# Performance work log

Hardware: AMD Instinct MI355X
Metric: run time of the kernel (lower is better)

The kernel has to match this reference:

```python
import jax, jax.numpy as jnp
import numpy as np

N = 50000      # nodes
E = 800000     # edges (avg degree 16)
D = 128        # embed_dim
H = 8          # nhead
HD = D // H    # head dim = 16


def setup_inputs() -> dict:
    key = jax.random.key(0)
    ks = jax.random.split(key, 6)
    s = 1.0 / np.sqrt(D)  # ~xavier scale for square matrices
    return {
        "feats": jax.random.normal(ks[0], (N, D), jnp.float32),
        "edge_index": jax.random.randint(ks[1], (E, 2), 0, N, dtype=jnp.int64),
        "Wq": jax.random.normal(ks[2], (D, D), jnp.float32) * s,
        "bq": jnp.zeros((D,), jnp.float32),
        "Wk": jax.random.normal(ks[3], (D, D), jnp.float32) * s,
        "bk": jnp.zeros((D,), jnp.float32),
        "Wv": jax.random.normal(ks[4], (D, D), jnp.float32) * s,
        "bv": jnp.zeros((D,), jnp.float32),
        "Wo": jax.random.normal(ks[5], (D, D), jnp.float32) * s,
        "bo": jnp.zeros((D,), jnp.float32),
    }


def reference(feats, edge_index, Wq, bq, Wk, bk, Wv, bv, Wo, bo):
    # Projections (nn.Linear: x @ W.T + b), split into heads: [N, H, HD]
    q = (feats @ Wq.T + bq).reshape(N, H, HD)
    k = (feats @ Wk.T + bk).reshape(N, H, HD)
    v = (feats @ Wv.T + bv).reshape(N, H, HD)

    r = edge_index[:, 0]  # source nodes
    c = edge_index[:, 1]  # destination nodes (softmax / aggregation groups)

    # Per-edge, per-head dot-product scores: [E, H]
    scores = jnp.einsum('ehd,ehd->eh', q[c], k[r]) / np.sqrt(HD)

    # Custom scatter-softmax: src_max clamped to min 0; extra exp(-src_max) in denom
    smax = jnp.maximum(jax.ops.segment_max(scores, c, num_segments=N), 0.0)  # [N, H]
    ex = jnp.exp(scores - smax[c])                                           # [E, H]
    denom = jax.ops.segment_sum(ex, c, num_segments=N)                       # [N, H]
    attn = ex / (denom + jnp.exp(-smax))[c]                                  # [E, H]

    # Weighted V per edge, scatter-mean to destination nodes
    out_e = attn[:, :, None] * v[r]                      # [E, H, HD]
    agg = jax.ops.segment_sum(out_e, c, num_segments=N)  # [N, H, HD]
    cnt = jax.ops.segment_sum(jnp.ones((E,), jnp.float32), c, num_segments=N)
    agg = agg / jnp.maximum(cnt, 1.0)[:, None, None]

    return agg.reshape(N, D) @ Wo.T + bo
```

## Files before the change

### kernel.cpp

```cpp
#include <hip/hip_runtime.h>
#include <hip/hip_bf16.h>

#define N_NODES 50000
#define N_EDGES 800000
#define DIM 128
#define NHEAD 8
#define HDIM 16
#define ELL_PAD 64
#define ELL_SLICES 391
#define ELL_BLOCKS (8 * ELL_SLICES)
#define ROWTILES 3125
#define QKV_WAVES (ROWTILES * 3)
#define QKV_GRID ((QKV_WAVES + 3) / 4)
#define OUT_WAVES (ROWTILES * 2)
#define OUT_GRID ((OUT_WAVES + 3) / 4)

#define Q_OFF      0ull
#define KV_OFF     12800000ull
#define AGG_OFF    38400000ull
#define ELL_OFF    51200000ull
#define CNT_OFF    64000000ull
#define WBF_OFF    64200192ull
#define BIAS_OFF   64331264ull

typedef __attribute__((ext_vector_type(8))) short short8;
typedef __attribute__((ext_vector_type(4))) float floatx4;

__device__ inline float bflo2f(unsigned u) { return __uint_as_float(u << 16); }
__device__ inline float bfhi2f(unsigned u) { return __uint_as_float(u & 0xffff0000u); }
__device__ inline unsigned short f2bf(float f) {
    unsigned u = __float_as_uint(f);
    return (unsigned short)((u + 0x7fffu + ((u >> 16) & 1u)) >> 16);
}

__device__ inline void detect_flags(const void* feats, const void* edge,
                                    int& isbf, int& is32) {
    const unsigned short* f = (const unsigned short*)feats;
    const unsigned int* eg = (const unsigned int*)edge;
    int lane = threadIdx.x & 63;
    unsigned e = (f[lane] >> 7) & 0xFF;
    int junk = (e >= 0x90 || (e > 0 && e <= 0x60)) ? 1 : 0;
    unsigned long long jm = __ballot(junk);
    int nz = (lane < 32 && eg[2 * lane + 1] != 0) ? 1 : 0;
    unsigned long long nm = __ballot(nz);
    isbf = (jm == 0ull) ? 1 : 0;
    is32 = (nm != 0ull) ? 1 : 0;
}

__device__ inline void load_edge(const int* edge, int is32, int e, int& r, int& c) {
    if (is32) { int2 p = ((const int2*)edge)[e]; r = p.x; c = p.y; }
    else {
        const long long* p = (const long long*)edge;
        r = (int)p[2 * e]; c = (int)p[2 * e + 1];
    }
    if ((unsigned)r >= N_NODES) r = 0;
    if ((unsigned)c >= N_NODES) c = 0;
}

__device__ inline float ldf(const void* p, int isbf, int i) {
    return isbf ? __bfloat162float(((const __hip_bfloat16*)p)[i])
                : ((const float*)p)[i];
}

__device__ inline short8 ldfrag(const void* base, int isbf, size_t off) {
    if (isbf) return *(const short8*)((const unsigned short*)base + off);
    const float* f = (const float*)base + off;
    float4 f0 = *(const float4*)f;
    float4 f1 = *(const float4*)(f + 4);
    short8 a;
    a[0] = (short)f2bf(f0.x); a[1] = (short)f2bf(f0.y);
    a[2] = (short)f2bf(f0.z); a[3] = (short)f2bf(f0.w);
    a[4] = (short)f2bf(f1.x); a[5] = (short)f2bf(f1.y);
    a[6] = (short)f2bf(f1.z); a[7] = (short)f2bf(f1.w);
    return a;
}

__global__ __launch_bounds__(256) void ell_build(const void* feats, const int* edge,
                                                 const void* wq, const void* wk,
                                                 const void* wv, const void* wo,
                                                 const void* bq, const void* bk,
                                                 const void* bv, const void* bo,
                                                 int* cnt, int* ell,
                                                 unsigned short* wbf, float* bias) {
    int isbf, is32; detect_flags(feats, edge, isbf, is32);

    if (blockIdx.x >= ELL_BLOCKS) {
        int b2 = blockIdx.x - ELL_BLOCKS;
        if (b2 == 256) {
            for (int j = threadIdx.x; j < 512; j += 256) {
                int m2 = j >> 7;
                const void* bb = (m2 == 0) ? bq : (m2 == 1) ? bk : (m2 == 2) ? bv : bo;
                bias[j] = ldf(bb, isbf, j & 127);
            }
            return;
        }
        if (isbf) return;
        int idx = b2 * 256 + (int)threadIdx.x;
        int mm = idx >> 14, rem = idx & 16383;
        const void* wsrc = (mm == 0) ? wq : (mm == 1) ? wk : (mm == 2) ? wv : wo;
        wbf[idx] = f2bf(((const float*)wsrc)[rem]);
        return;
    }

    int pid = blockIdx.x & 7, slice = blockIdx.x >> 3;
    int base = slice * 2048 + (int)threadIdx.x;
    #pragma unroll
    for (int j = 0; j < 8; ++j) {
        int e = base + j * 256;
        if (e < N_EDGES) {
            int r, c; load_edge(edge, is32, e, r, c);
            if ((c & 7) == pid) {
                int slot = atomicAdd(cnt + c, 1);
                if (slot < ELL_PAD) ell[c * ELL_PAD + slot] = r;
            }
        }
    }
}

__global__ __launch_bounds__(256) void qkv_mfma(const void* feats_raw, const int* edge,
                                                const void* wq_raw, const void* wk_raw,
                                                const void* wv_raw,
                                                const unsigned short* wbf,
                                                const float* bias,
                                                unsigned short* q_s, unsigned short* kv_s) {
    int isbf, is32; detect_flags(feats_raw, edge, isbf, is32);
    int w = blockIdx.x * 4 + (threadIdx.x >> 6);
    if (w >= QKV_WAVES) return;
    int rowtile = w / 3;
    int m = w - rowtile * 3;
    int lane = threadIdx.x & 63;
    int mrow = lane & 15, quad = lane >> 4;
    int arow = rowtile * 16 + mrow;

    short8 a[4];
    #pragma unroll
    for (int kt = 0; kt < 4; ++kt)
        a[kt] = ldfrag(feats_raw, isbf, (size_t)arow * DIM + quad * 8 + kt * 32);

    const void* wraw = (m == 0) ? wq_raw : (m == 1) ? wk_raw : wv_raw;
    const unsigned short* wm = isbf ? (const unsigned short*)wraw : wbf + m * 16384;
    int soff = (m == 2) ? 16 : 0;

    for (int nt = 0; nt < 8; ++nt) {
        float b = bias[m * 128 + nt * 16 + mrow];
        floatx4 acc = {b, b, b, b};
        const unsigned short* wp = wm + (size_t)(nt * 16 + mrow) * DIM + quad * 8;
        #pragma unroll
        for (int kt = 0; kt < 4; ++kt) {
            short8 bf = *(const short8*)(wp + kt * 32);
            acc = __builtin_amdgcn_mfma_f32_16x16x32_bf16(a[kt], bf, acc, 0, 0, 0);
        }
        if (m == 0) {
            #pragma unroll
            for (int r4 = 0; r4 < 4; ++r4) {
                int row = rowtile * 16 + quad * 4 + r4;
                q_s[(size_t)row * DIM + nt * 16 + mrow] = f2bf(acc[r4]);
            }
        } else {
            #pragma unroll
            for (int r4 = 0; r4 < 4; ++r4) {
                int row = rowtile * 16 + quad * 4 + r4;
                kv_s[(size_t)row * 256 + nt * 32 + soff + mrow] = f2bf(acc[r4]);
            }
        }
    }
}

__global__ __launch_bounds__(256) void node_agg(const int* __restrict__ cnt,
                                                const int* __restrict__ ell,
                                                const unsigned short* __restrict__ q_s,
                                                const uint4* __restrict__ kvpack,
                                                uint4* __restrict__ agg_bf) {
    int node = (blockIdx.x * 256 + threadIdx.x) >> 6;
    int lane = threadIdx.x & 63;
    if (node >= N_NODES) return;
    int e = lane >> 3, h = lane & 7;

    const uint4* qp = (const uint4*)(q_s + (size_t)node * DIM + h * HDIM);
    uint4 q0 = qp[0], q1 = qp[1];
    float qv[16];
    qv[0]  = bflo2f(q0.x); qv[1]  = bfhi2f(q0.x);
    qv[2]  = bflo2f(q0.y); qv[3]  = bfhi2f(q0.y);
    qv[4]  = bflo2f(q0.z); qv[5]  = bfhi2f(q0.z);
    qv[6]  = bflo2f(q0.w); qv[7]  = bfhi2f(q0.w);
    qv[8]  = bflo2f(q1.x); qv[9]  = bfhi2f(q1.x);
    qv[10] = bflo2f(q1.y); qv[11] = bfhi2f(q1.y);
    qv[12] = bflo2f(q1.z); qv[13] = bfhi2f(q1.z);
    qv[14] = bflo2f(q1.w); qv[15] = bfhi2f(q1.w);

    int degt = cnt[node];
    int deg = degt < ELL_PAD ? degt : ELL_PAD;
    float l = 0.f;
    float acc[16];
    #pragma unroll
    for (int i = 0; i < 16; ++i) acc[i] = 0.f;

    const int* erow = ell + node * ELL_PAD;
    for (int i0 = 0; i0 < deg; i0 += 16) {
        int i1 = i0 + e, i2 = i0 + 8 + e;
        bool ok1 = i1 < deg, ok2 = i2 < deg;
        int r1 = ok1 ? erow[i1] : 0;
        int r2 = ok2 ? erow[i2] : 0;
        const uint4* kp1 = kvpack + (size_t)r1 * 32 + h * 4;
        const uint4* kp2 = kvpack + (size_t)r2 * 32 + h * 4;
        uint4 ka1 = kp1[0], kb1 = kp1[1], va1 = kp1[2], vb1 = kp1[3];
        uint4 ka2 = kp2[0], kb2 = kp2[1], va2 = kp2[2], vb2 = kp2[3];

        float s1 = 0.f;
        s1 += bflo2f(ka1.x) * qv[0]  + bfhi2f(ka1.x) * qv[1];
        s1 += bflo2f(ka1.y) * qv[2]  + bfhi2f(ka1.y) * qv[3];
        s1 += bflo2f(ka1.z) * qv[4]  + bfhi2f(ka1.z) * qv[5];
        s1 += bflo2f(ka1.w) * qv[6]  + bfhi2f(ka1.w) * qv[7];
        s1 += bflo2f(kb1.x) * qv[8]  + bfhi2f(kb1.x) * qv[9];
        s1 += bflo2f(kb1.y) * qv[10] + bfhi2f(kb1.y) * qv[11];
        s1 += bflo2f(kb1.z) * qv[12] + bfhi2f(kb1.z) * qv[13];
        s1 += bflo2f(kb1.w) * qv[14] + bfhi2f(kb1.w) * qv[15];
        float p1 = ok1 ? __expf(s1 * 0.25f) : 0.f;
        l += p1;
        acc[0]  += p1 * bflo2f(va1.x); acc[1]  += p1 * bfhi2f(va1.x);
        acc[2]  += p1 * bflo2f(va1.y); acc[3]  += p1 * bfhi2f(va1.y);
        acc[4]  += p1 * bflo2f(va1.z); acc[5]  += p1 * bfhi2f(va1.z);
        acc[6]  += p1 * bflo2f(va1.w); acc[7]  += p1 * bfhi2f(va1.w);
        acc[8]  += p1 * bflo2f(vb1.x); acc[9]  += p1 * bfhi2f(vb1.x);
        acc[10] += p1 * bflo2f(vb1.y); acc[11] += p1 * bfhi2f(vb1.y);
        acc[12] += p1 * bflo2f(vb1.z); acc[13] += p1 * bfhi2f(vb1.z);
        acc[14] += p1 * bflo2f(vb1.w); acc[15] += p1 * bfhi2f(vb1.w);

        float s2 = 0.f;
        s2 += bflo2f(ka2.x) * qv[0]  + bfhi2f(ka2.x) * qv[1];
        s2 += bflo2f(ka2.y) * qv[2]  + bfhi2f(ka2.y) * qv[3];
        s2 += bflo2f(ka2.z) * qv[4]  + bfhi2f(ka2.z) * qv[5];
        s2 += bflo2f(ka2.w) * qv[6]  + bfhi2f(ka2.w) * qv[7];
        s2 += bflo2f(kb2.x) * qv[8]  + bfhi2f(kb2.x) * qv[9];
        s2 += bflo2f(kb2.y) * qv[10] + bfhi2f(kb2.y) * qv[11];
        s2 += bflo2f(kb2.z) * qv[12] + bfhi2f(kb2.z) * qv[13];
        s2 += bflo2f(kb2.w) * qv[14] + bfhi2f(kb2.w) * qv[15];
        float p2 = ok2 ? __expf(s2 * 0.25f) : 0.f;
        l += p2;
        acc[0]  += p2 * bflo2f(va2.x); acc[1]  += p2 * bfhi2f(va2.x);
        acc[2]  += p2 * bflo2f(va2.y); acc[3]  += p2 * bfhi2f(va2.y);
        acc[4]  += p2 * bflo2f(va2.z); acc[5]  += p2 * bfhi2f(va2.z);
        acc[6]  += p2 * bflo2f(va2.w); acc[7]  += p2 * bfhi2f(va2.w);
        acc[8]  += p2 * bflo2f(vb2.x); acc[9]  += p2 * bfhi2f(vb2.x);
        acc[10] += p2 * bflo2f(vb2.y); acc[11] += p2 * bfhi2f(vb2.y);
        acc[12] += p2 * bflo2f(vb2.z); acc[13] += p2 * bfhi2f(vb2.z);
        acc[14] += p2 * bflo2f(vb2.w); acc[15] += p2 * bfhi2f(vb2.w);
    }

    #pragma unroll
    for (int m = 8; m < 64; m <<= 1) {
        l += __shfl_xor(l, m);
        #pragma unroll
        for (int i = 0; i < 16; ++i) acc[i] += __shfl_xor(acc[i], m);
    }

    float inv = 1.0f / ((1.0f + l) * (float)(degt > 0 ? degt : 1));
    if (e == 0) {
        unsigned o[8];
        #pragma unroll
        for (int i = 0; i < 8; ++i)
            o[i] = (unsigned)f2bf(acc[2 * i] * inv) | ((unsigned)f2bf(acc[2 * i + 1] * inv) << 16);
        uint4* op = agg_bf + (size_t)node * 16 + h * 2;
        op[0] = make_uint4(o[0], o[1], o[2], o[3]);
        op[1] = make_uint4(o[4], o[5], o[6], o[7]);
    }
}

__global__ __launch_bounds__(256) void out_mfma(const unsigned short* agg_bf,
                                                const void* feats, const int* edge,
                                                const void* wo_raw,
                                                const unsigned short* wbf,
                                                const float* bias, void* out) {
    int isbf, is32; detect_flags(feats, edge, isbf, is32);
    const unsigned short* W = isbf ? (const unsigned short*)wo_raw : wbf + 3 * 16384;
    int w = blockIdx.x * 4 + (threadIdx.x >> 6);
    if (w >= OUT_WAVES) return;
    int rowtile = w >> 1;
    int nthalf = w & 1;
    int lane = threadIdx.x & 63;
    int mrow = lane & 15, quad = lane >> 4;
    int arow = rowtile * 16 + mrow;

    short8 a[4];
    const unsigned short* ap = agg_bf + (size_t)arow * DIM + quad * 8;
    #pragma unroll
    for (int kt = 0; kt < 4; ++kt) a[kt] = *(const short8*)(ap + kt * 32);

    for (int nt = nthalf * 4; nt < nthalf * 4 + 4; ++nt) {
        float b = bias[3 * 128 + nt * 16 + mrow];
        floatx4 acc = {b, b, b, b};
        const unsigned short* wp = W + (size_t)(nt * 16 + mrow) * DIM + quad * 8;
        #pragma unroll
        for (int kt = 0; kt < 4; ++kt) {
            short8 bf = *(const short8*)(wp + kt * 32);
            acc = __builtin_amdgcn_mfma_f32_16x16x32_bf16(a[kt], bf, acc, 0, 0, 0);
        }
        if (isbf) {
            #pragma unroll
            for (int r4 = 0; r4 < 4; ++r4) {
                int row = rowtile * 16 + quad * 4 + r4;
                ((unsigned short*)out)[(size_t)row * DIM + nt * 16 + mrow] = f2bf(acc[r4]);
            }
        } else {
            #pragma unroll
            for (int r4 = 0; r4 < 4; ++r4) {
                int row = rowtile * 16 + quad * 4 + r4;
                ((float*)out)[(size_t)row * DIM + nt * 16 + mrow] = acc[r4];
            }
        }
    }
}

extern "C" void kernel_launch(void* const* d_in, const int* in_sizes, int n_in,
                              void* d_out, int out_size, void* d_ws, size_t ws_size,
                              hipStream_t stream) {
    const void* feats = d_in[0];
    const int*  edge  = (const int*)d_in[1];
    const void* Wq = d_in[2]; const void* bq = d_in[3];
    const void* Wk = d_in[4]; const void* bk = d_in[5];
    const void* Wv = d_in[6]; const void* bv = d_in[7];
    const void* Wo = d_in[8]; const void* bo = d_in[9];

    char* ws = (char*)d_ws;
    unsigned short* q_s  = (unsigned short*)(ws + Q_OFF);
    unsigned short* kv_s = (unsigned short*)(ws + KV_OFF);
    unsigned short* aggb = (unsigned short*)(ws + AGG_OFF);
    int* ell             = (int*)(ws + ELL_OFF);
    int* cnt             = (int*)(ws + CNT_OFF);
    unsigned short* wbf  = (unsigned short*)(ws + WBF_OFF);
    float* bias          = (float*)(ws + BIAS_OFF);

    hipMemsetAsync(ws + CNT_OFF, 0, N_NODES * 4, stream);

    ell_build<<<ELL_BLOCKS + 257, 256, 0, stream>>>(feats, edge, Wq, Wk, Wv, Wo,
                                                    bq, bk, bv, bo, cnt, ell,
                                                    wbf, bias);

    qkv_mfma<<<QKV_GRID, 256, 0, stream>>>(feats, edge, Wq, Wk, Wv, wbf, bias,
                                           q_s, kv_s);

    node_agg<<<(N_NODES * 64 + 255) / 256, 256, 0, stream>>>(cnt, ell, q_s,
                                                             (const uint4*)(ws + KV_OFF),
                                                             (uint4*)aggb);

    out_mfma<<<OUT_GRID, 256, 0, stream>>>(aggb, feats, edge, Wo, wbf, bias, d_out);
}
```

Baseline: 257.7 us.

## Merge ELL build and QKV projection into one launch, convert weights inline

Combines the edge-bucketing kernel and the QKV MFMA projection into a single grid so the two independent phases run concurrently and one launch is removed. The separate fp32-to-bf16 weight and bias staging pass is dropped; each wave now converts weight fragments and reads bias directly from the raw inputs. Q/K/V stores become nontemporal. In exchange, every wave redoes the fp32 weight conversion in registers, which adds ALU work and doubles weight read bytes per fragment.

```diff
diff --git a/kernel.cpp b/kernel.cpp
--- a/kernel.cpp
+++ b/kernel.cpp
@@ -11,7 +11,7 @@
 #define ELL_BLOCKS (8 * ELL_SLICES)
 #define ROWTILES 3125
 #define QKV_WAVES (ROWTILES * 3)
-#define QKV_GRID ((QKV_WAVES + 3) / 4)
+#define QKV_BLOCKS ((QKV_WAVES + 3) / 4)
 #define OUT_WAVES (ROWTILES * 2)
 #define OUT_GRID ((OUT_WAVES + 3) / 4)
 
@@ -20,8 +20,6 @@
 #define AGG_OFF    38400000ull
 #define ELL_OFF    51200000ull
 #define CNT_OFF    64000000ull
-#define WBF_OFF    64200192ull
-#define BIAS_OFF   64331264ull
 
 typedef __attribute__((ext_vector_type(8))) short short8;
 typedef __attribute__((ext_vector_type(4))) float floatx4;
@@ -62,8 +60,7 @@
                 : ((const float*)p)[i];
 }
 
-__device__ inline short8 ldfrag(const void* base, int isbf, size_t off) {
-    if (isbf) return *(const short8*)((const unsigned short*)base + off);
+__device__ inline short8 ldfrag32(const void* base, size_t off) {
     const float* f = (const float*)base + off;
     float4 f0 = *(const float4*)f;
     float4 f1 = *(const float4*)(f + 4);
@@ -74,57 +71,38 @@
     a[6] = (short)f2bf(f1.z); a[7] = (short)f2bf(f1.w);
     return a;
 }
-
-__global__ __launch_bounds__(256) void ell_build(const void* feats, const int* edge,
-                                                 const void* wq, const void* wk,
-                                                 const void* wv, const void* wo,
-                                                 const void* bq, const void* bk,
-                                                 const void* bv, const void* bo,
-                                                 int* cnt, int* ell,
-                                                 unsigned short* wbf, float* bias) {
+__device__ inline short8 ldfrag(const void* base, int isbf, size_t off) {
+    if (isbf) return *(const short8*)((const unsigned short*)base + off);
+    return ldfrag32(base, off);
+}
+
+__global__ __launch_bounds__(256) void ell_qkv(const void* feats, const int* edge,
+                                               const void* wq, const void* wk,
+                                               const void* wv,
+                                               const void* bq, const void* bk,
+                                               const void* bv,
+                                               int* cnt, int* ell,
+                                               unsigned short* q_s, unsigned short* kv_s) {
     int isbf, is32; detect_flags(feats, edge, isbf, is32);
 
-    if (blockIdx.x >= ELL_BLOCKS) {
-        int b2 = blockIdx.x - ELL_BLOCKS;
-        if (b2 == 256) {
-            for (int j = threadIdx.x; j < 512; j += 256) {
-                int m2 = j >> 7;
-                const void* bb = (m2 == 0) ? bq : (m2 == 1) ? bk : (m2 == 2) ? bv : bo;
-                bias[j] = ldf(bb, isbf, j & 127);
-            }
-            return;
+    if (blockIdx.x < ELL_BLOCKS) {
+        int pid = blockIdx.x & 7, slice = blockIdx.x >> 3;
+        int base = slice * 2048 + (int)threadIdx.x;
+        #pragma unroll
+        for (int j = 0; j < 8; ++j) {
+            int e = base + j * 256;
+            if (e < N_EDGES) {
+                int r, c; load_edge(edge, is32, e, r, c);
+                if ((c & 7) == pid) {
+                    int slot = atomicAdd(cnt + c, 1);
+                    if (slot < ELL_PAD) ell[c * ELL_PAD + slot] = r;
+                }
+            }
         }
-        if (isbf) return;
-        int idx = b2 * 256 + (int)threadIdx.x;
-        int mm = idx >> 14, rem = idx & 16383;
-        const void* wsrc = (mm == 0) ? wq : (mm == 1) ? wk : (mm == 2) ? wv : wo;
-        wbf[idx] = f2bf(((const float*)wsrc)[rem]);
         return;
     }
 
-    int pid = blockIdx.x & 7, slice = blockIdx.x >> 3;
-    int base = slice * 2048 + (int)threadIdx.x;
-    #pragma unroll
-    for (int j = 0; j < 8; ++j) {
-        int e = base + j * 256;
-        if (e < N_EDGES) {
-            int r, c; load_edge(edge, is32, e, r, c);
-            if ((c & 7) == pid) {
-                int slot = atomicAdd(cnt + c, 1);
-                if (slot < ELL_PAD) ell[c * ELL_PAD + slot] = r;
-            }
-        }
-    }
-}
-
-__global__ __launch_bounds__(256) void qkv_mfma(const void* feats_raw, const int* edge,
-                                                const void* wq_raw, const void* wk_raw,
-                                                const void* wv_raw,
-                                                const unsigned short* wbf,
-                                                const float* bias,
-                                                unsigned short* q_s, unsigned short* kv_s) {
-    int isbf, is32; detect_flags(feats_raw, edge, isbf, is32);
-    int w = blockIdx.x * 4 + (threadIdx.x >> 6);
+    int w = (blockIdx.x - ELL_BLOCKS) * 4 + (threadIdx.x >> 6);
     if (w >= QKV_WAVES) return;
     int rowtile = w / 3;
     int m = w - rowtile * 3;
@@ -135,32 +113,43 @@
     short8 a[4];
     #pragma unroll
     for (int kt = 0; kt < 4; ++kt)
-        a[kt] = ldfrag(feats_raw, isbf, (size_t)arow * DIM + quad * 8 + kt * 32);
-
-    const void* wraw = (m == 0) ? wq_raw : (m == 1) ? wk_raw : wv_raw;
-    const unsigned short* wm = isbf ? (const unsigned short*)wraw : wbf + m * 16384;
+        a[kt] = ldfrag(feats, isbf, (size_t)arow * DIM + quad * 8 + kt * 32);
+
+    const void* wraw = (m == 0) ? wq : (m == 1) ? wk : wv;
+    const void* braw = (m == 0) ? bq : (m == 1) ? bk : bv;
     int soff = (m == 2) ? 16 : 0;
 
     for (int nt = 0; nt < 8; ++nt) {
-        float b = bias[m * 128 + nt * 16 + mrow];
+        float b = ldf(braw, isbf, nt * 16 + mrow);
         floatx4 acc = {b, b, b, b};
-        const unsigned short* wp = wm + (size_t)(nt * 16 + mrow) * DIM + quad * 8;
-        #pragma unroll
-        for (int kt = 0; kt < 4; ++kt) {
-            short8 bf = *(const short8*)(wp + kt * 32);
-            acc = __builtin_amdgcn_mfma_f32_16x16x32_bf16(a[kt], bf, acc, 0, 0, 0);
+        if (isbf) {
+            const unsigned short* wp = (const unsigned short*)wraw +
+                                       (size_t)(nt * 16 + mrow) * DIM + quad * 8;
+            #pragma unroll
+            for (int kt = 0; kt < 4; ++kt) {
+                short8 bf = *(const short8*)(wp + kt * 32);
+                acc = __builtin_amdgcn_mfma_f32_16x16x32_bf16(a[kt], bf, acc, 0, 0, 0);
+            }
+        } else {
+            #pragma unroll
+            for (int kt = 0; kt < 4; ++kt) {
+                short8 bf = ldfrag32(wraw, (size_t)(nt * 16 + mrow) * DIM + quad * 8 + kt * 32);
+                acc = __builtin_amdgcn_mfma_f32_16x16x32_bf16(a[kt], bf, acc, 0, 0, 0);
+            }
         }
         if (m == 0) {
             #pragma unroll
             for (int r4 = 0; r4 < 4; ++r4) {
                 int row = rowtile * 16 + quad * 4 + r4;
-                q_s[(size_t)row * DIM + nt * 16 + mrow] = f2bf(acc[r4]);
+                __builtin_nontemporal_store(f2bf(acc[r4]),
+                    q_s + (size_t)row * DIM + nt * 16 + mrow);
             }
         } else {
             #pragma unroll
             for (int r4 = 0; r4 < 4; ++r4) {
                 int row = rowtile * 16 + quad * 4 + r4;
-                kv_s[(size_t)row * 256 + nt * 32 + soff + mrow] = f2bf(acc[r4]);
+                __builtin_nontemporal_store(f2bf(acc[r4]),
+                    kv_s + (size_t)row * 256 + nt * 32 + soff + mrow);
             }
         }
     }
@@ -268,11 +257,9 @@
 
 __global__ __launch_bounds__(256) void out_mfma(const unsigned short* agg_bf,
                                                 const void* feats, const int* edge,
-                                                const void* wo_raw,
-                                                const unsigned short* wbf,
-                                                const float* bias, void* out) {
+                                                const void* wo_raw, const void* bo,
+                                                void* out) {
     int isbf, is32; detect_flags(feats, edge, isbf, is32);
-    const unsigned short* W = isbf ? (const unsigned short*)wo_raw : wbf + 3 * 16384;
     int w = blockIdx.x * 4 + (threadIdx.x >> 6);
     if (w >= OUT_WAVES) return;
     int rowtile = w >> 1;
@@ -287,21 +274,27 @@
     for (int kt = 0; kt < 4; ++kt) a[kt] = *(const short8*)(ap + kt * 32);
 
     for (int nt = nthalf * 4; nt < nthalf * 4 + 4; ++nt) {
-        float b = bias[3 * 128 + nt * 16 + mrow];
+        float b = ldf(bo, isbf, nt * 16 + mrow);
         floatx4 acc = {b, b, b, b};
-        const unsigned short* wp = W + (size_t)(nt * 16 + mrow) * DIM + quad * 8;
-        #pragma unroll
-        for (int kt = 0; kt < 4; ++kt) {
-            short8 bf = *(const short8*)(wp + kt * 32);
-            acc = __builtin_amdgcn_mfma_f32_16x16x32_bf16(a[kt], bf, acc, 0, 0, 0);
-        }
         if (isbf) {
+            const unsigned short* wp = (const unsigned short*)wo_raw +
+                                       (size_t)(nt * 16 + mrow) * DIM + quad * 8;
+            #pragma unroll
+            for (int kt = 0; kt < 4; ++kt) {
+                short8 bf = *(const short8*)(wp + kt * 32);
+                acc = __builtin_amdgcn_mfma_f32_16x16x32_bf16(a[kt], bf, acc, 0, 0, 0);
+            }
             #pragma unroll
             for (int r4 = 0; r4 < 4; ++r4) {
                 int row = rowtile * 16 + quad * 4 + r4;
                 ((unsigned short*)out)[(size_t)row * DIM + nt * 16 + mrow] = f2bf(acc[r4]);
             }
         } else {
+            #pragma unroll
+            for (int kt = 0; kt < 4; ++kt) {
+                short8 bf = ldfrag32(wo_raw, (size_t)(nt * 16 + mrow) * DIM + quad * 8 + kt * 32);
+                acc = __builtin_amdgcn_mfma_f32_16x16x32_bf16(a[kt], bf, acc, 0, 0, 0);
+            }
             #pragma unroll
             for (int r4 = 0; r4 < 4; ++r4) {
                 int row = rowtile * 16 + quad * 4 + r4;
@@ -327,21 +320,16 @@
     unsigned short* aggb = (unsigned short*)(ws + AGG_OFF);
     int* ell             = (int*)(ws + ELL_OFF);
     int* cnt             = (int*)(ws + CNT_OFF);
-    unsigned short* wbf  = (unsigned short*)(ws + WBF_OFF);
-    float* bias          = (float*)(ws + BIAS_OFF);
 
     hipMemsetAsync(ws + CNT_OFF, 0, N_NODES * 4, stream);
 
-    ell_build<<<ELL_BLOCKS + 257, 256, 0, stream>>>(feats, edge, Wq, Wk, Wv, Wo,
-                                                    bq, bk, bv, bo, cnt, ell,
-                                                    wbf, bias);
-
-    qkv_mfma<<<QKV_GRID, 256, 0, stream>>>(feats, edge, Wq, Wk, Wv, wbf, bias,
-                                           q_s, kv_s);
+    ell_qkv<<<ELL_BLOCKS + QKV_BLOCKS, 256, 0, stream>>>(feats, edge, Wq, Wk, Wv,
+                                                         bq, bk, bv, cnt, ell,
+                                                         q_s, kv_s);
 
     node_agg<<<(N_NODES * 64 + 255) / 256, 256, 0, stream>>>(cnt, ell, q_s,
                                                              (const uint4*)(ws + KV_OFF),
                                                              (uint4*)aggb);
 
-    out_mfma<<<OUT_GRID, 256, 0, stream>>>(aggb, feats, edge, Wo, wbf, bias, d_out);
-}
+    out_mfma<<<OUT_GRID, 256, 0, stream>>>(aggb, feats, edge, Wo, bo, d_out);
+}
```

Result: slower. 299.3 us (+16.1%).
